# Kernel tuning notes

Measured on AMD Instinct MI355X. Metric: run time of the kernel, lower is better.

## Reference

```python
import jax, jax.numpy as jnp
import numpy as np

B, D, TOPC = 8, 1024, 256
CIN, DOWN, BR, NR, G = 64, 128, 2, 8, 8
GC = DOWN // G
H = W = 64
LN_EPS = 1e-5


def _ln(x, g, b):
    mu = x.mean(-1, keepdims=True)
    var = ((x - mu) ** 2).mean(-1, keepdims=True)
    return (x - mu) * jax.lax.rsqrt(var + LN_EPS) * g + b


def _gelu(x):
    return jax.nn.gelu(x, approximate=False)


def _sample_topleft(I, IX, IY, IT, x, y):
    # x, y: [B, N] continuous coords; returns [B, CIN, N]
    x = x[:, None, :]
    y = y[:, None, :]
    X = jnp.ceil(x).astype(jnp.int32)
    Y = jnp.ceil(y).astype(jnp.int32)
    z = jnp.zeros_like(X)
    dx = X - x
    dy = Y - y
    b = jnp.arange(B)[:, None, None]
    c = jnp.arange(CIN)[None, :, None]
    wx1 = 0.5 * dx ** 2
    wx2 = dx - wx1
    wy1 = 0.5 * dy ** 2
    wy2 = dy - wy1
    s_a = IT[b, c, X, Y]
    s_e1 = (wy1 * (IX[b, c, X, Y - 1] - 0.5 * I[b, c, X, Y - 1] - 0.5 * I[b, c, z, Y - 1])
            + wy2 * (IX[b, c, X, Y] - 0.5 * I[b, c, X, Y] - 0.5 * I[b, c, z, Y]))
    s_e2 = (wx1 * (IY[b, c, X - 1, Y] - 0.5 * I[b, c, X - 1, Y] - 0.5 * I[b, c, X - 1, z])
            + wx2 * (IY[b, c, X, Y] - 0.5 * I[b, c, X, Y] - 0.5 * I[b, c, X, z]))
    s_c = (wx1 * wy1 * I[b, c, X - 1, Y - 1] + wx2 * wy1 * I[b, c, X, Y - 1]
           + wx1 * wy2 * I[b, c, X - 1, Y] + wx2 * wy2 * I[b, c, X, Y])
    return s_a - s_e1 - s_e2 + s_c


def setup_inputs() -> dict:
    key = jax.random.key(0)
    ks = jax.random.split(key, 20)
    s = 0.02
    return {
        "x": jax.random.normal(ks[0], (B, D, TOPC), jnp.float32),
        "I": jax.random.normal(ks[1], (B, CIN, H, W), jnp.float32),
        "IX": jax.random.normal(ks[2], (B, CIN, H, W), jnp.float32),
        "IY": jax.random.normal(ks[3], (B, CIN, H, W), jnp.float32),
        "IT": jax.random.normal(ks[4], (B, CIN, H, W), jnp.float32),
        "w_idx": jax.random.normal(ks[5], (BR * NR * 4, TOPC), jnp.float32) * s,
        "b_idx": jnp.zeros((BR * NR * 4,), jnp.float32),
        "w_proj": jax.random.normal(ks[6], (DOWN, CIN), jnp.float32) * s,
        "b_proj": jnp.zeros((DOWN,), jnp.float32),
        "w_mask": jax.random.normal(ks[7], (BR * NR * G, TOPC), jnp.float32) * s,
        "b_mask": jnp.zeros((BR * NR * G,), jnp.float32),
        "g1": jnp.ones((DOWN,), jnp.float32),
        "beta1": jnp.zeros((DOWN,), jnp.float32),
        "w_mlp1": jax.random.normal(ks[8], (4 * DOWN, DOWN), jnp.float32) * s,
        "b_mlp1": jnp.zeros((4 * DOWN,), jnp.float32),
        "w_mlp2": jax.random.normal(ks[9], (DOWN, 4 * DOWN), jnp.float32) * s,
        "b_mlp2": jnp.zeros((DOWN,), jnp.float32),
        "g2": jnp.ones((DOWN,), jnp.float32),
        "beta2": jnp.zeros((DOWN,), jnp.float32),
    }


def reference(x, I, IX, IY, IT, w_idx, b_idx, w_proj, b_proj, w_mask, b_mask,
              g1, beta1, w_mlp1, b_mlp1, w_mlp2, b_mlp2, g2, beta2):
    # rect prediction
    p = x @ w_idx.T + b_idx                       # [B, D, BR*NR*4]
    fac = jnp.array([H - 1, W - 1, H - 1, W - 1], jnp.float32)
    p = jax.nn.sigmoid(p.reshape(B, D, BR, NR, 4)) * fac
    p = p.reshape(B, D * BR * NR, 4)
    x1, y1, x2, y2 = p[:, :, 0], p[:, :, 1], p[:, :, 2], p[:, :, 3]
    S = (_sample_topleft(I, IX, IY, IT, x2, y2)
         - _sample_topleft(I, IX, IY, IT, x1, y2)
         - _sample_topleft(I, IX, IY, IT, x2, y1)
         + _sample_topleft(I, IX, IY, IT, x1, y1))  # [B, CIN, N]
    S = S.reshape(B, CIN, D, BR, NR).transpose(0, 2, 3, 4, 1)  # [B, D, BR, NR, CIN]
    rects = _gelu(S @ w_proj.T + b_proj)           # [B, D, BR, NR, DOWN]
    mask = (x @ w_mask.T + b_mask).reshape(B, D * BR, NR, G, 1)
    mask = jax.nn.softmax(mask, axis=2)
    rects = rects.reshape(B, D * BR, NR, G, GC)
    out = (mask * rects).sum(2).reshape(B, D * BR, DOWN)
    out = _ln(out, g1, beta1)
    shortcut = out
    out = _gelu(out @ w_mlp1.T + b_mlp1) @ w_mlp2.T + b_mlp2
    return _ln(out, g2, beta2) + shortcut
```

## Files before the change

kernel.cpp:

```cpp
#include <hip/hip_runtime.h>
#include <hip/hip_bf16.h>
#include <hip/hip_fp16.h>
#include <math.h>

#define BB   8
#define DD   1024

typedef short bh8 __attribute__((ext_vector_type(8)));
typedef float f32x4 __attribute__((ext_vector_type(4)));
typedef _Float16 h2f __attribute__((ext_vector_type(2)));

__device__ __forceinline__ ushort f2bf(float f) {
    uint u = __builtin_bit_cast(uint, f);
    u += 0x7fffu + ((u >> 16) & 1u);
    return (ushort)(u >> 16);
}
__device__ __forceinline__ float asf(uint u)  { return __builtin_bit_cast(float, u); }
__device__ __forceinline__ float bflo(uint u) { return __builtin_bit_cast(float, u << 16); }
__device__ __forceinline__ float bfhi(uint u) { return __builtin_bit_cast(float, u & 0xffff0000u); }
__device__ __forceinline__ uint  pkh(float a, float b) {
    return __builtin_bit_cast(uint, __builtin_amdgcn_cvt_pkrtz(a, b));
}
__device__ __forceinline__ h2f ash2f(uint u) { return __builtin_bit_cast(h2f, u); }

#if __has_builtin(__builtin_amdgcn_fdot2)
__device__ __forceinline__ float fdot2h(h2f a, h2f b, float c) {
    return __builtin_amdgcn_fdot2(a, b, c, false);
}
#else
__device__ __forceinline__ float fdot2h(h2f a, h2f b, float c) {
    return fmaf((float)a.x, (float)b.x, fmaf((float)a.y, (float)b.y, c));
}
#endif

__device__ __forceinline__ uint cvtpk_bf16(float a, float b) {
    uint r;
    asm("v_cvt_pk_bf16_f32 %0, %1, %2" : "=v"(r) : "v"(a), "v"(b));
    return r;
}
__device__ __forceinline__ ushort cvt1_bf16(float a) {
    uint r;
    asm("v_cvt_pk_bf16_f32 %0, %1, %2" : "=v"(r) : "v"(a), "v"(a));
    return (ushort)r;
}

__device__ __forceinline__ float gelu_fast(float x) {
    float x2 = x * x;
#if __has_builtin(__builtin_amdgcn_exp2f)
    float e = __builtin_amdgcn_exp2f(x * fmaf(x2, -0.20588652f, -2.3022082f));
#else
    float e = __expf(-(1.5957691216f * x + 0.14270963f * x * x2));
#endif
    return x * __builtin_amdgcn_rcpf(1.0f + e);
}
__device__ __forceinline__ float sig63(float v) {
    return 63.0f * __builtin_amdgcn_rcpf(1.0f + __expf(-v));
}

__global__ __launch_bounds__(256) void kT_pack(
    const float* __restrict__ w_idx, const float* __restrict__ w_mask,
    const float* __restrict__ w_proj, const float* __restrict__ w1,
    const float* __restrict__ w2,
    ushort* __restrict__ catPh, ushort* __restrict__ catPm,
    ushort* __restrict__ catPl,
    ushort* __restrict__ w_projP, ushort* __restrict__ w1P,
    ushort* __restrict__ w2P, uint* __restrict__ rowflag)
{
    int bid = blockIdx.x, t = threadIdx.x;
    if (bid < 24) {
        int gid = bid * 256 + t;
        int l = gid & 63, ks = (gid >> 6) & 7, nt = gid >> 9;
        int n = nt * 16 + (l & 15);
        int kbase = ks * 32 + ((l >> 4) << 3);
        const float* src = (n < 64) ? (w_idx + (size_t)n * 256)
                                    : (w_mask + (size_t)(n - 64) * 256);
        ushort* dh = catPh + (size_t)gid * 8;
        ushort* dm = catPm + (size_t)gid * 8;
        ushort* dl = catPl + (size_t)gid * 8;
        #pragma unroll
        for (int j = 0; j < 8; ++j) {
            float v = src[kbase + j];
            ushort h = f2bf(v);
            float hf = __builtin_bit_cast(float, (uint)h << 16);
            float r1 = v - hf;
            ushort m = f2bf(r1); float mf = __builtin_bit_cast(float, (uint)m << 16);
            ushort lo = f2bf(r1 - mf);
            dh[j] = h; dm[j] = m; dl[j] = lo;
        }
    } else if (bid < 28) {
        int g = (bid - 24) * 256 + t;
        int nt = g >> 7, ks = (g >> 6) & 1, l = g & 63;
        int n = nt * 16 + (l & 15), k0 = ks * 32 + (l >> 4) * 8;
        ushort* dst = w_projP + (size_t)g * 8;
        #pragma unroll
        for (int j = 0; j < 8; ++j) dst[j] = f2bf(w_proj[n * 64 + k0 + j]);
    } else if (bid < 60) {
        int g = (bid - 28) * 256 + t;
        int nt = g >> 8, ks = (g >> 6) & 3, l = g & 63;
        int n = nt * 16 + (l & 15), k0 = ks * 32 + (l >> 4) * 8;
        ushort* dst = w1P + (size_t)g * 8;
        #pragma unroll
        for (int j = 0; j < 8; ++j) dst[j] = f2bf(w1[n * 128 + k0 + j]);
    } else if (bid < 92) {
        int g = (bid - 60) * 256 + t;
        int nt = g >> 10, ks = (g >> 6) & 15, l = g & 63;
        int n = nt * 16 + (l & 15), k0 = ks * 32 + (l >> 4) * 8;
        ushort* dst = w2P + (size_t)g * 8;
        #pragma unroll
        for (int j = 0; j < 8; ++j) dst[j] = f2bf(w2[n * 512 + k0 + j]);
    } else {
        if (t < 128) rowflag[t] = 0u;
    }
}

__global__ __launch_bounds__(256) void kA_coords(
    const float* __restrict__ x,
    const ushort* __restrict__ catPh, const ushort* __restrict__ catPm,
    const ushort* __restrict__ catPl,
    const float* __restrict__ b_idx, const float* __restrict__ b_mask,
    float* __restrict__ maskw, float* __restrict__ coords,
    unsigned char* __restrict__ rowflag)
{
    __shared__ __align__(16) float sOut[16 * 193];
    int t = threadIdx.x;
    int bb8 = blockIdx.x & 7, jj = blockIdx.x >> 3;
    size_t rowbase = ((size_t)bb8 * 64 + (size_t)jj) * 16;
    int w = t >> 6, l = t & 63;

    f32x4 acc[3];
    acc[0] = (f32x4){0.f,0.f,0.f,0.f};
    acc[1] = (f32x4){0.f,0.f,0.f,0.f};
    acc[2] = (f32x4){0.f,0.f,0.f,0.f};
    const float* xr = x + (rowbase + (size_t)(l & 15)) * 256 + ((l >> 4) << 3);

    #pragma unroll
    for (int half = 0; half < 2; ++half) {
        bh8 Ah[4], Am[4], Al[4];
        #pragma unroll
        for (int k4 = 0; k4 < 4; ++k4) {
            int ks = half * 4 + k4;
            float4 v0 = *(const float4*)(xr + ks * 32);
            float4 v1 = *(const float4*)(xr + ks * 32 + 4);
            uint4 uh, um, ul;
            uh.x = cvtpk_bf16(v0.x, v0.y);
            uh.y = cvtpk_bf16(v0.z, v0.w);
            uh.z = cvtpk_bf16(v1.x, v1.y);
            uh.w = cvtpk_bf16(v1.z, v1.w);
            float r0a = v0.x - bflo(uh.x), r0b = v0.y - bfhi(uh.x);
            float r0c = v0.z - bflo(uh.y), r0d = v0.w - bfhi(uh.y);
            float r1a = v1.x - bflo(uh.z), r1b = v1.y - bfhi(uh.z);
            float r1c = v1.z - bflo(uh.w), r1d = v1.w - bfhi(uh.w);
            um.x = cvtpk_bf16(r0a, r0b);
            um.y = cvtpk_bf16(r0c, r0d);
            um.z = cvtpk_bf16(r1a, r1b);
            um.w = cvtpk_bf16(r1c, r1d);
            ul.x = cvtpk_bf16(r0a - bflo(um.x), r0b - bfhi(um.x));
            ul.y = cvtpk_bf16(r0c - bflo(um.y), r0d - bfhi(um.y));
            ul.z = cvtpk_bf16(r1a - bflo(um.z), r1b - bfhi(um.z));
            ul.w = cvtpk_bf16(r1c - bflo(um.w), r1d - bfhi(um.w));
            Ah[k4] = __builtin_bit_cast(bh8, uh);
            Am[k4] = __builtin_bit_cast(bh8, um);
            Al[k4] = __builtin_bit_cast(bh8, ul);
        }
        #pragma unroll
        for (int ntl = 0; ntl < 3; ++ntl) {
            int nt = w * 3 + ntl;
            #pragma unroll
            for (int k4 = 0; k4 < 4; ++k4) {
                int ks = half * 4 + k4;
                size_t fo = ((size_t)(nt * 8 + ks) * 64 + l) * 8;
                bh8 bh = *(const bh8*)(catPh + fo);
                bh8 bm = *(const bh8*)(catPm + fo);
                bh8 bl = *(const bh8*)(catPl + fo);
                acc[ntl] = __builtin_amdgcn_mfma_f32_16x16x32_bf16(Ah[k4], bh, acc[ntl], 0, 0, 0);
                acc[ntl] = __builtin_amdgcn_mfma_f32_16x16x32_bf16(Ah[k4], bm, acc[ntl], 0, 0, 0);
                acc[ntl] = __builtin_amdgcn_mfma_f32_16x16x32_bf16(Am[k4], bh, acc[ntl], 0, 0, 0);
                acc[ntl] = __builtin_amdgcn_mfma_f32_16x16x32_bf16(Ah[k4], bl, acc[ntl], 0, 0, 0);
                acc[ntl] = __builtin_amdgcn_mfma_f32_16x16x32_bf16(Al[k4], bh, acc[ntl], 0, 0, 0);
                acc[ntl] = __builtin_amdgcn_mfma_f32_16x16x32_bf16(Am[k4], bm, acc[ntl], 0, 0, 0);
            }
        }
    }
    {
        int r0 = (l >> 4) * 4, cbase = w * 48 + (l & 15);
        #pragma unroll
        for (int ntl = 0; ntl < 3; ++ntl)
            #pragma unroll
            for (int reg = 0; reg < 4; ++reg)
                sOut[(r0 + reg) * 193 + cbase + ntl * 16] = acc[ntl][reg];
    }
    __syncthreads();

    {
        int row = t >> 4, u = t & 15;
        const float* so = sOut + row * 193;
        int br = u >> 3, nr = u & 7;
        int c0 = br * 32 + nr * 4;
        float4 co;
        co.x = sig63(so[c0 + 0] + b_idx[c0 + 0]);
        co.y = sig63(so[c0 + 1] + b_idx[c0 + 1]);
        co.z = sig63(so[c0 + 2] + b_idx[c0 + 2]);
        co.w = sig63(so[c0 + 3] + b_idx[c0 + 3]);
        size_t tile = rowbase + row;
        *(float4*)(coords + (tile * 16 + (size_t)u) * 4) = co;
        int bb = (int)(tile >> 10);
        int Xa = (int)ceilf(co.x); Xa = Xa < 1 ? 1 : (Xa > 63 ? 63 : Xa);
        int Xb = (int)ceilf(co.z); Xb = Xb < 1 ? 1 : (Xb > 63 ? 63 : Xb);
        rowflag[bb * 64 + Xa] = 1;
        rowflag[bb * 64 + Xb] = 1;
    }
    {
        int row = t >> 4, br = (t >> 3) & 1, g = t & 7;
        const float* so = sOut + row * 193 + 64;
        float lg[8];
        float mx = -1e30f;
        #pragma unroll
        for (int nr = 0; nr < 8; ++nr) {
            int idx = br * 64 + nr * 8 + g;
            lg[nr] = so[idx] + b_mask[idx];
            mx = fmaxf(mx, lg[nr]);
        }
        float s = 0.f;
        #pragma unroll
        for (int nr = 0; nr < 8; ++nr) { lg[nr] = __expf(lg[nr] - mx); s += lg[nr]; }
        float inv = __builtin_amdgcn_rcpf(s);
        #pragma unroll
        for (int nr = 0; nr < 8; ++nr)
            maskw[(rowbase + row) * 128 + br * 64 + nr * 8 + g] = lg[nr] * inv;
    }
}

__global__ __launch_bounds__(256) void kB_tex(
    const float* __restrict__ I, const float* __restrict__ IX,
    const float* __restrict__ IY, const float* __restrict__ IT,
    const unsigned char* __restrict__ rowflag,
    uint4* __restrict__ T1, ushort* __restrict__ T2)
{
    __shared__ __align__(16) float sf[6528];
    int t = threadIdx.x;
    int bid = blockIdx.x;
    int b = bid & 7, r = bid >> 3;
    int chunk = r & 3, h = r >> 2;
    if (rowflag[b * 64 + h] == 0) return;

    int hp = h > 0 ? h - 1 : 0;
    int cb = chunk * 16;
    size_t inb  = (size_t)b * 262144 + (size_t)h  * 64;
    size_t inbp = (size_t)b * 262144 + (size_t)hp * 64;

    {
        int c = t >> 4, w4 = (t & 15) << 2;
        size_t o = (size_t)(cb + c) * 4096 + w4;
        int so = c * 68 + w4;
        *(float4*)(sf + 0 * 1088 + so) = *(const float4*)(I  + inb  + o);
        *(float4*)(sf + 1 * 1088 + so) = *(const float4*)(I  + inbp + o);
        *(float4*)(sf + 2 * 1088 + so) = *(const float4*)(IX + inb  + o);
        *(float4*)(sf + 3 * 1088 + so) = *(const float4*)(IY + inb  + o);
        *(float4*)(sf + 4 * 1088 + so) = *(const float4*)(IY + inbp + o);
        *(float4*)(sf + 5 * 1088 + so) = *(const float4*)(IT + inb  + o);
    }
    __syncthreads();

    #pragma unroll
    for (int i = 0; i < 4; ++i) {
        int idx = i * 256 + t; int w = idx >> 4, c = idx & 15;
        int wm = w > 0 ? w - 1 : 0;
        int rb = c * 68;
        float I00 = sf[rb + w],        I0m = sf[rb + wm];
        float Im0 = sf[1088 + rb + w], Imm = sf[1088 + rb + wm];
        float E1  = sf[2176 + rb + w]  - 0.5f * I00;
        float E1m = sf[2176 + rb + wm] - 0.5f * I0m;
        float E2  = sf[3264 + rb + w]  - 0.5f * I00;
        float E2m = sf[4352 + rb + w]  - 0.5f * Im0;
        float v0 = sf[5440 + rb + w];
        float v1 = -E1;
        float v2 = 0.5f * (E1 - E1m);
        float v3 = -E2;
        float v4 = 0.5f * (E2 - E2m);
        float v5 = I00;
        float v6 = 0.5f * (I0m - I00);
        float v7 = 0.5f * (Im0 - I00);
        float v8 = 0.25f * ((Imm - I0m) - (Im0 - I00));
        size_t pt = (((size_t)b * 4096) + (size_t)h * 64 + w) * 64 + (cb + c);
        uint4 o4;
        o4.x = pkh(v0, v1);
        o4.y = pkh(v2, v3);
        o4.z = pkh(v4, v5);
        o4.w = pkh(v6, v7);
        T1[pt] = o4;
        T2[pt] = (ushort)(pkh(v8, 0.f) & 0xffffu);
    }
}

__global__ __launch_bounds__(256) void k2_rects(
    const uint4* __restrict__ T1, const ushort* __restrict__ T2,
    const float* __restrict__ coords,
    const ushort* __restrict__ w_projP, const float* __restrict__ b_proj,
    const float* __restrict__ maskw, const float* __restrict__ g1,
    const float* __restrict__ beta1, float* __restrict__ mid)
{
    __shared__ __align__(16) uint meta_lds[16][32];
    __shared__ __align__(16) float S_lds[16][68];
    __shared__ float mrow[128];
    __shared__ float outr[2][128];
    int bid = blockIdx.x;
    int b = bid & 7, d = bid >> 3;
    int t = threadIdx.x, w = t >> 6, l = t & 63;
    size_t tile = (size_t)b * DD + d;
    if (t < 64) {
        int u = t >> 2, c = t & 3;
        float4 co = *(const float4*)(coords + (tile * 16 + (size_t)u) * 4);
        float x1 = co.x, y1 = co.y, x2 = co.z, y2 = co.w;
        int X1 = (int)ceilf(x1); X1 = X1 < 1 ? 1 : (X1 > 63 ? 63 : X1);
        int X2 = (int)ceilf(x2); X2 = X2 < 1 ? 1 : (X2 > 63 ? 63 : X2);
        int Y1 = (int)ceilf(y1); Y1 = Y1 < 1 ? 1 : (Y1 > 63 ? 63 : Y1);
        int Y2 = (int)ceilf(y2); Y2 = Y2 < 1 ? 1 : (Y2 > 63 ? 63 : Y2);
        float dxa = (float)X1 - x1, dxb = (float)X2 - x2;
        float dya = (float)Y1 - y1, dyb = (float)Y2 - y2;
        int   Xc = (c & 1) ? X1 : X2;
        int   Yc = (c < 2) ? Y2 : Y1;
        float s  = (c == 0 || c == 3) ? 1.f : -1.f;
        float dx = (c & 1) ? dxa : dxb;
        float dy = (c < 2) ? dyb : dya;
        float dx2 = dx * dx, dy2 = dy * dy;
        uint pt = (uint)(Xc * 64 + Yc);
        uint4 wa, wb;
        wa.x = pt * 1024u;
        wa.y = pt * 128u;
        wa.z = pkh(s, s * dy);
        wa.w = pkh(s * dy2, s * dx);
        wb.x = pkh(s * dx2, s * dx * dy);
        wb.y = pkh(s * dx * dy2, s * dx2 * dy);
        wb.z = __builtin_bit_cast(uint, s * dx2 * dy2);
        wb.w = 0u;
        *(uint4*)&meta_lds[u][c * 8 + 0] = wa;
        *(uint4*)&meta_lds[u][c * 8 + 4] = wb;
    }
    if (t >= 128) mrow[t - 128] = maskw[tile * 128 + (t - 128)];

    bh8 bf[2][2];
    #pragma unroll
    for (int ni = 0; ni < 2; ++ni) {
        int nt = w * 2 + ni;
        #pragma unroll
        for (int ks = 0; ks < 2; ++ks)
            bf[ni][ks] = *(const bh8*)(w_projP + ((size_t)(nt * 2 + ks) * 64 + l) * 8);
    }
    __syncthreads();
    const char* t1b = ((const char*)T1) + ((size_t)b << 22) + (size_t)(l * 16);
    const char* t2b = ((const char*)T2) + ((size_t)b << 19) + (size_t)(l * 2);

    int m0 = w * 4;
    uint4 q[2][4]; ushort e8[2][4];
    #pragma unroll
    for (int g = 0; g < 2; ++g) {
        #pragma unroll
        for (int c = 0; c < 4; ++c) {
            uint o1 = __builtin_amdgcn_readfirstlane(meta_lds[m0 + g][c * 8 + 0]);
            uint o2 = __builtin_amdgcn_readfirstlane(meta_lds[m0 + g][c * 8 + 1]);
            q[g][c]  = *(const uint4*)(t1b + o1);
            e8[g][c] = *(const ushort*)(t2b + o2);
        }
    }
    #pragma unroll
    for (int rr = 0; rr < 4; ++rr) {
        int m = m0 + rr;
        int cur = rr & 1;
        uint4 qc[4]; ushort ec[4];
        #pragma unroll
        for (int c = 0; c < 4; ++c) { qc[c] = q[cur][c]; ec[c] = e8[cur][c]; }
        if (rr < 2) {
            int mn = m + 2;
            #pragma unroll
            for (int c = 0; c < 4; ++c) {
                uint o1 = __builtin_amdgcn_readfirstlane(meta_lds[mn][c * 8 + 0]);
                uint o2 = __builtin_amdgcn_readfirstlane(meta_lds[mn][c * 8 + 1]);
                q[cur][c]  = *(const uint4*)(t1b + o1);
                e8[cur][c] = *(const ushort*)(t2b + o2);
            }
        }
        float acc0 = 0.f, acc1 = 0.f;
        #pragma unroll
        for (int c = 0; c < 4; ++c) {
            uint cz = meta_lds[m][c * 8 + 2], cw = meta_lds[m][c * 8 + 3];
            uint bx = meta_lds[m][c * 8 + 4], by = meta_lds[m][c * 8 + 5];
            float bz = asf(meta_lds[m][c * 8 + 6]);
            float ev = __half2float(__builtin_bit_cast(__half, ec[c]));
            float cv = bz * ev;
            cv = fdot2h(ash2f(by), ash2f(qc[c].w), cv);
            cv = fdot2h(ash2f(bx), ash2f(qc[c].z), cv);
            cv = fdot2h(ash2f(cw), ash2f(qc[c].y), cv);
            cv = fdot2h(ash2f(cz), ash2f(qc[c].x), cv);
            if (c & 1) acc1 += cv; else acc0 += cv;
        }
        S_lds[m][l] = acc0 + acc1;
    }
    __syncthreads();

    int am = l & 15, q2 = l >> 4;
    bh8 a0, a1;
    {
        float4 va = *(const float4*)&S_lds[am][q2 * 8];
        float4 vb = *(const float4*)&S_lds[am][q2 * 8 + 4];
        uint4 ua;
        ua.x = cvtpk_bf16(va.x, va.y);
        ua.y = cvtpk_bf16(va.z, va.w);
        ua.z = cvtpk_bf16(vb.x, vb.y);
        ua.w = cvtpk_bf16(vb.z, vb.w);
        a0 = __builtin_bit_cast(bh8, ua);
        float4 vc = *(const float4*)&S_lds[am][32 + q2 * 8];
        float4 vd = *(const float4*)&S_lds[am][32 + q2 * 8 + 4];
        uint4 ub;
        ub.x = cvtpk_bf16(vc.x, vc.y);
        ub.y = cvtpk_bf16(vc.z, vc.w);
        ub.z = cvtpk_bf16(vd.x, vd.y);
        ub.w = cvtpk_bf16(vd.z, vd.w);
        a1 = __builtin_bit_cast(bh8, ub);
    }
    f32x4 cc[2];
    cc[0] = (f32x4){0.f, 0.f, 0.f, 0.f};
    cc[1] = (f32x4){0.f, 0.f, 0.f, 0.f};
    cc[0] = __builtin_amdgcn_mfma_f32_16x16x32_bf16(a0, bf[0][0], cc[0], 0, 0, 0);
    cc[0] = __builtin_amdgcn_mfma_f32_16x16x32_bf16(a1, bf[0][1], cc[0], 0, 0, 0);
    cc[1] = __builtin_amdgcn_mfma_f32_16x16x32_bf16(a0, bf[1][0], cc[1], 0, 0, 0);
    cc[1] = __builtin_amdgcn_mfma_f32_16x16x32_bf16(a1, bf[1][1], cc[1], 0, 0, 0);

    int cl = l & 15;
    #pragma unroll
    for (int ni = 0; ni < 2; ++ni) {
        int nt = w * 2 + ni;
        int col = nt * 16 + cl;
        float bpv = b_proj[col];
        float p = 0.f;
        #pragma unroll
        for (int reg = 0; reg < 4; ++reg) {
            int r = q2 * 4 + reg;
            float v = cc[ni][reg] + bpv;
            p += gelu_fast(v) * mrow[(r >> 3) * 64 + (r & 7) * 8 + nt];
        }
        p += __shfl_xor(p, 16, 64);
        if (q2 == 0) outr[0][col] = p;
        else if (q2 == 2) outr[1][col] = p;
    }
    __syncthreads();

    if (w < 2) {
        float v0 = outr[w][l], v1 = outr[w][l + 64];
        float s = v0 + v1, sq = v0 * v0 + v1 * v1;
        #pragma unroll
        for (int mm = 32; mm > 0; mm >>= 1) {
            s  += __shfl_xor(s, mm, 64);
            sq += __shfl_xor(sq, mm, 64);
        }
        float mu  = s * (1.0f / 128.0f);
        float var = sq * (1.0f / 128.0f) - mu * mu;
        float rs  = rsqrtf(var + 1e-5f);
        size_t ob = (tile * 2 + w) * 128;
        mid[ob + l]      = (v0 - mu) * rs * g1[l]      + beta1[l];
        mid[ob + l + 64] = (v1 - mu) * rs * g1[l + 64] + beta1[l + 64];
    }
}

__global__ __launch_bounds__(256) void k4_mlp(
    const float* __restrict__ mid, const ushort* __restrict__ w1P,
    const float* __restrict__ b1, const ushort* __restrict__ w2P,
    const float* __restrict__ b2, const float* __restrict__ g2,
    const float* __restrict__ beta2, float* __restrict__ outp)
{
    __shared__ float xr[16][132];
    __shared__ __align__(16) ushort Af[4][64][8];
    __shared__ __align__(16) ushort H[16][520];
    __shared__ float oo[16][128];
    __shared__ float b1s[512];
    __shared__ float b2s[128], g2s[128], bt2s[128];
    int t = threadIdx.x, w = t >> 6, l = t & 63;
    int bid = blockIdx.x;
    int mt = (bid & 7) * 128 + (bid >> 3);
    size_t rowbase = (size_t)mt * 16;

    {
        const float4* mg = (const float4*)(mid + rowbase * 128);
        #pragma unroll
        for (int i4 = 0; i4 < 2; ++i4) {
            int i = i4 * 256 + t;
            float4 v = mg[i];
            *(float4*)(&xr[i >> 5][(i & 31) * 4]) = v;
        }
    }
    for (int i = t; i < 512; i += 256) b1s[i] = b1[i];
    if (t < 128) { b2s[t] = b2[t]; g2s[t] = g2[t]; bt2s[t] = beta2[t]; }
    __syncthreads();

    {
        int ks = t >> 6, m = l & 15, c0 = ks * 32 + (l >> 4) * 8;
        uint* dst = (uint*)&Af[ks][l][0];
        #pragma unroll
        for (int j = 0; j < 4; ++j)
            dst[j] = cvtpk_bf16(xr[m][c0 + 2 * j], xr[m][c0 + 2 * j + 1]);
    }
    __syncthreads();

    f32x4 c1[8];
    #pragma unroll
    for (int i = 0; i < 8; ++i) c1[i] = (f32x4){0.f, 0.f, 0.f, 0.f};
    bh8 a[4];
    #pragma unroll
    for (int ks = 0; ks < 4; ++ks) a[ks] = *(const bh8*)&Af[ks][l][0];
    #pragma unroll
    for (int ni = 0; ni < 8; ++ni) {
        int nt = w * 8 + ni;
        #pragma unroll
        for (int ks = 0; ks < 4; ++ks) {
            bh8 bfr = *(const bh8*)(w1P + ((size_t)(nt * 4 + ks) * 64 + l) * 8);
            c1[ni] = __builtin_amdgcn_mfma_f32_16x16x32_bf16(a[ks], bfr, c1[ni], 0, 0, 0);
        }
    }
    #pragma unroll
    for (int ni = 0; ni < 8; ++ni) {
        int nt = w * 8 + ni;
        int col = nt * 16 + (l & 15);
        int r0 = (l >> 4) * 4;
        #pragma unroll
        for (int reg = 0; reg < 4; ++reg)
            H[r0 + reg][col] = cvt1_bf16(gelu_fast(c1[ni][reg] + b1s[col]));
    }
    __syncthreads();

    f32x4 c2[2];
    c2[0] = (f32x4){0.f, 0.f, 0.f, 0.f};
    c2[1] = (f32x4){0.f, 0.f, 0.f, 0.f};
    const char* hb = (const char*)&H[0][0];
    #pragma unroll
    for (int ks2 = 0; ks2 < 16; ++ks2) {
        bh8 af = *(const bh8*)(hb + (l & 15) * 1040 + ks2 * 64 + (l >> 4) * 16);
        #pragma unroll
        for (int i = 0; i < 2; ++i) {
            int nt2 = w * 2 + i;
            bh8 bfr = *(const bh8*)(w2P + ((size_t)(nt2 * 16 + ks2) * 64 + l) * 8);
            c2[i] = __builtin_amdgcn_mfma_f32_16x16x32_bf16(af, bfr, c2[i], 0, 0, 0);
        }
    }
    #pragma unroll
    for (int i = 0; i < 2; ++i) {
        int col = (w * 2 + i) * 16 + (l & 15);
        int r0 = (l >> 4) * 4;
        #pragma unroll
        for (int reg = 0; reg < 4; ++reg) oo[r0 + reg][col] = c2[i][reg] + b2s[col];
    }
    __syncthreads();

    #pragma unroll
    for (int rr = 0; rr < 4; ++rr) {
        int r = w * 4 + rr;
        float v0 = oo[r][l], v1 = oo[r][l + 64];
        float s = v0 + v1, sq = v0 * v0 + v1 * v1;
        #pragma unroll
        for (int m = 32; m > 0; m >>= 1) {
            s  += __shfl_xor(s, m, 64);
            sq += __shfl_xor(sq, m, 64);
        }
        float mu  = s * (1.0f / 128.0f);
        float var = sq * (1.0f / 128.0f) - mu * mu;
        float rs  = rsqrtf(var + 1e-5f);
        size_t ob = (rowbase + r) * 128;
        outp[ob + l]      = (v0 - mu) * rs * g2s[l]      + bt2s[l]      + xr[r][l];
        outp[ob + l + 64] = (v1 - mu) * rs * g2s[l + 64] + bt2s[l + 64] + xr[r][l + 64];
    }
}

extern "C" void kernel_launch(void* const* d_in, const int* in_sizes, int n_in,
                              void* d_out, int out_size, void* d_ws, size_t ws_size,
                              hipStream_t stream) {
    const float* x      = (const float*)d_in[0];
    const float* I      = (const float*)d_in[1];
    const float* IX     = (const float*)d_in[2];
    const float* IY     = (const float*)d_in[3];
    const float* IT     = (const float*)d_in[4];
    const float* w_idx  = (const float*)d_in[5];
    const float* b_idx  = (const float*)d_in[6];
    const float* w_proj = (const float*)d_in[7];
    const float* b_proj = (const float*)d_in[8];
    const float* w_mask = (const float*)d_in[9];
    const float* b_mask = (const float*)d_in[10];
    const float* g1     = (const float*)d_in[11];
    const float* beta1  = (const float*)d_in[12];
    const float* w_mlp1 = (const float*)d_in[13];
    const float* b_mlp1 = (const float*)d_in[14];
    const float* w_mlp2 = (const float*)d_in[15];
    const float* b_mlp2 = (const float*)d_in[16];
    const float* g2     = (const float*)d_in[17];
    const float* beta2  = (const float*)d_in[18];
    float* out = (float*)d_out;

    float* ws = (float*)d_ws;
    ushort* catPh  = (ushort*)ws;
    ushort* catPm  = (ushort*)(ws + 24576);
    ushort* catPl  = (ushort*)(ws + 49152);
    ushort* w_projP = (ushort*)(ws + 73728);
    ushort* w1P     = (ushort*)(ws + 77824);
    ushort* w2P     = (ushort*)(ws + 110592);
    float*  maskw   = ws + 143360;
    float*  coords  = ws + 1191936;
    uint4*  T1      = (uint4*)(ws + 1716224);
    ushort* T2      = (ushort*)(ws + 10104832);
    unsigned char* rowflag = (unsigned char*)(ws + 11153408);

    kT_pack<<<93, 256, 0, stream>>>(w_idx, w_mask, w_proj, w_mlp1, w_mlp2,
                                    catPh, catPm, catPl, w_projP, w1P, w2P,
                                    (uint*)rowflag);
    kA_coords<<<512, 256, 0, stream>>>(x, catPh, catPm, catPl, b_idx, b_mask,
                                       maskw, coords, rowflag);
    kB_tex<<<2048, 256, 0, stream>>>(I, IX, IY, IT, rowflag, T1, T2);
    k2_rects<<<8192, 256, 0, stream>>>(T1, T2, coords, w_projP, b_proj, maskw,
                                       g1, beta1, out);
    k4_mlp<<<1024, 256, 0, stream>>>(out, w1P, b_mlp1, w2P, b_mlp2, g2, beta2, out);
}
```

Baseline: 78.55 us.

## Skip texture precompute for unreferenced points and deepen gather prefetch to three rows

Adds a per-batch 64x64 point occupancy bitmap filled in the coordinate kernel from the four rounded corners of each rectangle. The texture-precompute kernel then skips computing and storing entries for (h,w) points no sample touches, going beyond the existing per-row skip. Separately, the rect kernel's gather prefetch now issues three rows of loads up front instead of two, trading more registers for more memory latency hiding. The risk is correctness if samples read neighbours (X-1, Y-1) whose entries were never written, or if the corner-to-entry mapping misses some accessed point.

```diff
diff --git a/kernel.cpp b/kernel.cpp
--- a/kernel.cpp
+++ b/kernel.cpp
@@ -64,7 +64,8 @@
     ushort* __restrict__ catPh, ushort* __restrict__ catPm,
     ushort* __restrict__ catPl,
     ushort* __restrict__ w_projP, ushort* __restrict__ w1P,
-    ushort* __restrict__ w2P, uint* __restrict__ rowflag)
+    ushort* __restrict__ w2P, uint* __restrict__ rowflag,
+    uint* __restrict__ pointflag)
 {
     int bid = blockIdx.x, t = threadIdx.x;
     if (bid < 24) {
@@ -108,8 +109,10 @@
         ushort* dst = w2P + (size_t)g * 8;
         #pragma unroll
         for (int j = 0; j < 8; ++j) dst[j] = f2bf(w2[n * 512 + k0 + j]);
+    } else if (bid == 92) {
+        if (t < 128) rowflag[t] = 0u;
     } else {
-        if (t < 128) rowflag[t] = 0u;
+        pointflag[(bid - 93) * 256 + t] = 0u;
     }
 }
 
@@ -119,7 +122,7 @@
     const ushort* __restrict__ catPl,
     const float* __restrict__ b_idx, const float* __restrict__ b_mask,
     float* __restrict__ maskw, float* __restrict__ coords,
-    unsigned char* __restrict__ rowflag)
+    unsigned char* __restrict__ rowflag, unsigned char* __restrict__ pointflag)
 {
     __shared__ __align__(16) float sOut[16 * 193];
     int t = threadIdx.x;
@@ -206,8 +209,15 @@
         int bb = (int)(tile >> 10);
         int Xa = (int)ceilf(co.x); Xa = Xa < 1 ? 1 : (Xa > 63 ? 63 : Xa);
         int Xb = (int)ceilf(co.z); Xb = Xb < 1 ? 1 : (Xb > 63 ? 63 : Xb);
+        int Ya = (int)ceilf(co.y); Ya = Ya < 1 ? 1 : (Ya > 63 ? 63 : Ya);
+        int Yb = (int)ceilf(co.w); Yb = Yb < 1 ? 1 : (Yb > 63 ? 63 : Yb);
         rowflag[bb * 64 + Xa] = 1;
         rowflag[bb * 64 + Xb] = 1;
+        unsigned char* pf = pointflag + bb * 4096;
+        pf[Xa * 64 + Ya] = 1;
+        pf[Xa * 64 + Yb] = 1;
+        pf[Xb * 64 + Ya] = 1;
+        pf[Xb * 64 + Yb] = 1;
     }
     {
         int row = t >> 4, br = (t >> 3) & 1, g = t & 7;
@@ -234,6 +244,7 @@
     const float* __restrict__ I, const float* __restrict__ IX,
     const float* __restrict__ IY, const float* __restrict__ IT,
     const unsigned char* __restrict__ rowflag,
+    const unsigned char* __restrict__ pointflag,
     uint4* __restrict__ T1, ushort* __restrict__ T2)
 {
     __shared__ __align__(16) float sf[6528];
@@ -247,6 +258,7 @@
     int cb = chunk * 16;
     size_t inb  = (size_t)b * 262144 + (size_t)h  * 64;
     size_t inbp = (size_t)b * 262144 + (size_t)hp * 64;
+    const unsigned char* pf = pointflag + b * 4096 + h * 64;
 
     {
         int c = t >> 4, w4 = (t & 15) << 2;
@@ -264,6 +276,7 @@
     #pragma unroll
     for (int i = 0; i < 4; ++i) {
         int idx = i * 256 + t; int w = idx >> 4, c = idx & 15;
+        if (pf[w] == 0) continue;
         int wm = w > 0 ? w - 1 : 0;
         int rb = c * 68;
         float I00 = sf[rb + w],        I0m = sf[rb + wm];
@@ -351,9 +364,9 @@
     const char* t2b = ((const char*)T2) + ((size_t)b << 19) + (size_t)(l * 2);
 
     int m0 = w * 4;
-    uint4 q[2][4]; ushort e8[2][4];
-    #pragma unroll
-    for (int g = 0; g < 2; ++g) {
+    uint4 q[3][4]; ushort e8[3][4];
+    #pragma unroll
+    for (int g = 0; g < 3; ++g) {
         #pragma unroll
         for (int c = 0; c < 4; ++c) {
             uint o1 = __builtin_amdgcn_readfirstlane(meta_lds[m0 + g][c * 8 + 0]);
@@ -365,18 +378,18 @@
     #pragma unroll
     for (int rr = 0; rr < 4; ++rr) {
         int m = m0 + rr;
-        int cur = rr & 1;
+        int cur = (rr < 3) ? rr : 0;
         uint4 qc[4]; ushort ec[4];
         #pragma unroll
         for (int c = 0; c < 4; ++c) { qc[c] = q[cur][c]; ec[c] = e8[cur][c]; }
-        if (rr < 2) {
-            int mn = m + 2;
+        if (rr == 0) {
+            int mn = m0 + 3;
             #pragma unroll
             for (int c = 0; c < 4; ++c) {
                 uint o1 = __builtin_amdgcn_readfirstlane(meta_lds[mn][c * 8 + 0]);
                 uint o2 = __builtin_amdgcn_readfirstlane(meta_lds[mn][c * 8 + 1]);
-                q[cur][c]  = *(const uint4*)(t1b + o1);
-                e8[cur][c] = *(const ushort*)(t2b + o2);
+                q[0][c]  = *(const uint4*)(t1b + o1);
+                e8[0][c] = *(const ushort*)(t2b + o2);
             }
         }
         float acc0 = 0.f, acc1 = 0.f;
@@ -603,14 +616,15 @@
     float*  coords  = ws + 1191936;
     uint4*  T1      = (uint4*)(ws + 1716224);
     ushort* T2      = (ushort*)(ws + 10104832);
-    unsigned char* rowflag = (unsigned char*)(ws + 11153408);
-
-    kT_pack<<<93, 256, 0, stream>>>(w_idx, w_mask, w_proj, w_mlp1, w_mlp2,
-                                    catPh, catPm, catPl, w_projP, w1P, w2P,
-                                    (uint*)rowflag);
+    unsigned char* rowflag   = (unsigned char*)(ws + 11153408);
+    unsigned char* pointflag = (unsigned char*)(ws + 11153536);
+
+    kT_pack<<<125, 256, 0, stream>>>(w_idx, w_mask, w_proj, w_mlp1, w_mlp2,
+                                     catPh, catPm, catPl, w_projP, w1P, w2P,
+                                     (uint*)rowflag, (uint*)pointflag);
     kA_coords<<<512, 256, 0, stream>>>(x, catPh, catPm, catPl, b_idx, b_mask,
-                                       maskw, coords, rowflag);
-    kB_tex<<<2048, 256, 0, stream>>>(I, IX, IY, IT, rowflag, T1, T2);
+                                       maskw, coords, rowflag, pointflag);
+    kB_tex<<<2048, 256, 0, stream>>>(I, IX, IY, IT, rowflag, pointflag, T1, T2);
     k2_rects<<<8192, 256, 0, stream>>>(T1, T2, coords, w_projP, b_proj, maskw,
                                        g1, beta1, out);
     k4_mlp<<<1024, 256, 0, stream>>>(out, w1P, b_mlp1, w2P, b_mlp2, g2, beta2, out);
```

Measured after the change: 78.89 us. No clear change (+0.4%).
